# Optimization experiments

Measured on AMD Instinct MI355X. Metric: run time of the kernel, lower is better.

## Reference

```python
import jax, jax.numpy as jnp
import numpy as np
from jax import lax

EPS = 1e-5


def fps(xyz, npoint):
    # Farthest point sampling; xyz [B, N, 3] -> idx [B, npoint] (starts at point 0)
    B, N, _ = xyz.shape

    def body(carry, _):
        dist, far = carry
        c = jnp.take_along_axis(xyz, far[:, None, None], axis=1)  # [B,1,3]
        d = jnp.sum((xyz - c) ** 2, -1)                            # [B,N]
        dist = jnp.minimum(dist, d)
        nxt = jnp.argmax(dist, -1).astype(jnp.int32)
        return (dist, nxt), far

    init = (jnp.full((B, N), 1e10, xyz.dtype), jnp.zeros((B,), jnp.int32))
    _, idx = lax.scan(body, init, None, length=npoint)
    return idx.T  # [B, npoint]


def query_ball(radius, nsample, xyz, new_xyz):
    # xyz [B,N,3], new_xyz [B,S,3] -> idx [B,S,nsample]
    N = xyz.shape[1]
    sqr = jnp.sum((new_xyz[:, :, None, :] - xyz[:, None, :, :]) ** 2, -1)  # [B,S,N]
    idx = jnp.where(sqr > radius * radius, N, jnp.arange(N)[None, None, :])
    idx = jnp.sort(idx, axis=-1)[:, :, :nsample]
    # out-of-ball slots get replaced by the first in-ball index (torch repo behavior)
    return jnp.where(idx == N, idx[:, :, :1], idx)


def gather_pts(x, idx):
    # x [B,N,C], idx [B,...] -> [B,...,C]
    B = x.shape[0]
    b = jnp.arange(B).reshape((B,) + (1,) * (idx.ndim - 1))
    return x[b, idx]


def mlp_bn(x, layers):
    # x [B,S,K,C]; shared 1x1-conv MLP + training-mode BatchNorm + ReLU
    for w, g, b in layers:
        x = jnp.einsum('bskc,oc->bsko', x, w)
        mean = x.mean((0, 1, 2))
        var = x.var((0, 1, 2))  # biased, as torch BN uses for normalization
        x = jax.nn.relu((x - mean) * lax.rsqrt(var + EPS) * g + b)
    return x


def set_abstraction(xyz, points, npoint, radius, nsample, layers, group_all):
    B = xyz.shape[0]
    if group_all:
        new_xyz = jnp.zeros((B, 1, 3), xyz.dtype)
        new_points = xyz[:, None]  # [B,1,N,3] (raw xyz, no centering)
        if points is not None:
            new_points = jnp.concatenate([new_points, points[:, None]], -1)
    else:
        fidx = fps(xyz, npoint)
        new_xyz = gather_pts(xyz, fidx)                     # [B,S,3]
        idx = query_ball(radius, nsample, xyz, new_xyz)     # [B,S,K]
        grouped = gather_pts(xyz, idx) - new_xyz[:, :, None, :]
        if points is not None:
            new_points = jnp.concatenate([grouped, gather_pts(points, idx)], -1)
        else:
            new_points = grouped
    feat = mlp_bn(new_points, layers).max(2)  # max-pool over neighbors -> [B,S,C]
    return new_xyz, feat


def _forward(xyz_time, l1, l2, l3):
    B, T, N, _ = xyz_time.shape
    x = xyz_time.reshape(B * T, N, 4)
    xyz, t = x[..., :3], x[..., 3:]
    x1_xyz, x1 = set_abstraction(xyz, t, 512, 0.2, 32, l1, False)
    x2_xyz, x2 = set_abstraction(x1_xyz, x1, 128, 0.4, 64, l2, False)
    _, x3 = set_abstraction(x2_xyz, x2, None, None, None, l3, True)
    return x3.reshape(B, T, -1)


def setup_inputs() -> dict:
    key = jax.random.key(0)
    ks = jax.random.split(key, 16)
    inp = {"xyz_time": jax.random.uniform(ks[0], (2, 4, 4096, 4), jnp.float32)}
    specs = {1: [(64, 4), (64, 64), (128, 64)],
             2: [(128, 131), (128, 128), (256, 128)],
             3: [(256, 259), (512, 256), (1024, 512)]}
    i = 1
    for s, layers in specs.items():
        for j, (o, c) in enumerate(layers):
            inp[f"w{s}_{j}"] = jax.random.normal(jax.random.fold_in(ks[i], j), (o, c), jnp.float32) * 0.1
            inp[f"g{s}_{j}"] = jnp.ones((o,), jnp.float32)
            inp[f"b{s}_{j}"] = jnp.zeros((o,), jnp.float32)
        i += 1
    return inp


def reference(xyz_time, w1_0, g1_0, b1_0, w1_1, g1_1, b1_1, w1_2, g1_2, b1_2,
              w2_0, g2_0, b2_0, w2_1, g2_1, b2_1, w2_2, g2_2, b2_2,
              w3_0, g3_0, b3_0, w3_1, g3_1, b3_1, w3_2, g3_2, b3_2):
    l1 = [(w1_0, g1_0, b1_0), (w1_1, g1_1, b1_1), (w1_2, g1_2, b1_2)]
    l2 = [(w2_0, g2_0, b2_0), (w2_1, g2_1, b2_1), (w2_2, g2_2, b2_2)]
    l3 = [(w3_0, g3_0, b3_0), (w3_1, g3_1, b3_1), (w3_2, g3_2, b3_2)]
    return _forward(xyz_time, l1, l2, l3)
```

## Files before the change

kernel.cpp:

```cpp
#include <hip/hip_runtime.h>


typedef short s16x8 __attribute__((ext_vector_type(8)));
typedef float f32x4 __attribute__((ext_vector_type(4)));

__device__ __forceinline__ unsigned short f2bf_rne(float f) {
    unsigned u = __float_as_uint(f);
    u += 0x7FFFu + ((u >> 16) & 1u);
    return (unsigned short)(u >> 16);
}
__device__ __forceinline__ void f2bf_split(float v, unsigned short& hi,
                                           unsigned short& lo) {
    unsigned u = __float_as_uint(v);
    unsigned r = u + 0x7FFFu + ((u >> 16) & 1u);
    hi = (unsigned short)(r >> 16);
    float vh = __uint_as_float(r & 0xFFFF0000u);
    lo = f2bf_rne(v - vh);
}

__device__ __forceinline__ unsigned long long umax64(unsigned long long a,
                                                     unsigned long long b) {
    return a > b ? a : b;
}

__device__ __forceinline__ unsigned wred_umax63(unsigned v) {
    unsigned t;
    t = (unsigned)__builtin_amdgcn_update_dpp(0, (int)v, 0x111, 0xf, 0xf, true); if (t > v) v = t;
    t = (unsigned)__builtin_amdgcn_update_dpp(0, (int)v, 0x112, 0xf, 0xf, true); if (t > v) v = t;
    t = (unsigned)__builtin_amdgcn_update_dpp(0, (int)v, 0x114, 0xf, 0xf, true); if (t > v) v = t;
    t = (unsigned)__builtin_amdgcn_update_dpp(0, (int)v, 0x118, 0xf, 0xf, true); if (t > v) v = t;
    t = (unsigned)__builtin_amdgcn_update_dpp(0, (int)v, 0x142, 0xa, 0xf, true); if (t > v) v = t;
    t = (unsigned)__builtin_amdgcn_update_dpp(0, (int)v, 0x143, 0xc, 0xf, true); if (t > v) v = t;
    return v;
}

__device__ __forceinline__ void wave_argmax(unsigned dbits, unsigned nInv,
                                            unsigned& vmax, unsigned& iInv) {
    unsigned m = wred_umax63(dbits);
    vmax = (unsigned)__builtin_amdgcn_readlane((int)m, 63);
    unsigned cand = (dbits == vmax) ? nInv : 0u;
    unsigned im = wred_umax63(cand);
    iInv = (unsigned)__builtin_amdgcn_readlane((int)im, 63);
}

template<int NT, int ITEMS, int STRIDE>
__global__ __launch_bounds__(NT) void fps_block(
    const float* __restrict__ pts, int npoint,
    int* __restrict__ outIdx, float* __restrict__ outXyz)
{
    constexpr int N = NT * ITEMS;
    constexpr int NW = NT / 64;
    __shared__ float4 scoord[N];
    __shared__ unsigned long long wkey[2][NW];

    const int b = blockIdx.x;
    const int tid = threadIdx.x;
    const int wid = tid >> 6;
    const int lane = tid & 63;
    const float* P = pts + (size_t)b * N * STRIDE;

    float px[ITEMS], py[ITEMS], pz[ITEMS], dloc[ITEMS];
#pragma unroll
    for (int w = 0; w < ITEMS; ++w) {
        int n = tid + w * NT;
        float x, y, z;
        if (STRIDE == 4) {
            float4 v = *(const float4*)(P + (size_t)n * 4);
            x = v.x; y = v.y; z = v.z;
        } else {
            x = P[(size_t)n * STRIDE + 0];
            y = P[(size_t)n * STRIDE + 1];
            z = P[(size_t)n * STRIDE + 2];
        }
        px[w] = x; py[w] = y; pz[w] = z;
        scoord[n] = make_float4(x, y, z, 0.f);
        dloc[w] = 1e10f;
    }
    __syncthreads();
    float4 c0 = scoord[0];
    float cx = c0.x, cy = c0.y, cz = c0.z;
    int far = 0;

    for (int i = 0; i < npoint; ++i) {
        if (tid == 0) {
            outIdx[(size_t)b * npoint + i] = far;
            outXyz[((size_t)b * npoint + i) * 3 + 0] = cx;
            outXyz[((size_t)b * npoint + i) * 3 + 1] = cy;
            outXyz[((size_t)b * npoint + i) * 3 + 2] = cz;
        }
        float bestV = -1.0f;
        int bestW = 0;
#pragma unroll
        for (int w = 0; w < ITEMS; ++w) {
            float dx = __fsub_rn(px[w], cx);
            float dy = __fsub_rn(py[w], cy);
            float dz = __fsub_rn(pz[w], cz);
            float d = __fadd_rn(__fadd_rn(__fmul_rn(dx, dx), __fmul_rn(dy, dy)),
                                __fmul_rn(dz, dz));
            float dd = fminf(dloc[w], d);
            dloc[w] = dd;
            if (dd > bestV) { bestV = dd; bestW = w; }
        }
        int bestN = tid + bestW * NT;
        unsigned vmax, iInv;
        wave_argmax(__float_as_uint(bestV), 0xFFFFFFFFu ^ (unsigned)bestN,
                    vmax, iInv);
        const int par = i & 1;
        if (lane == 0)
            wkey[par][wid] = ((unsigned long long)vmax << 32) | iInv;
        __syncthreads();
        unsigned long long kb = wkey[par][0];
#pragma unroll
        for (int w2 = 1; w2 < NW; ++w2) kb = umax64(kb, wkey[par][w2]);
        far = (int)(0xFFFFFFFFu ^ (unsigned)kb);
        float4 cc = scoord[far];
        cx = cc.x; cy = cc.y; cz = cc.z;
    }
}

template<int ITEMS, int STRIDE>
__global__ __launch_bounds__(64) void fps_wave(
    const float* __restrict__ pts, int npoint,
    int* __restrict__ outIdx, float* __restrict__ outXyz)
{
    constexpr int N = 64 * ITEMS;
    __shared__ float4 scoord[N];

    const int b = blockIdx.x;
    const int tid = threadIdx.x;
    const float* P = pts + (size_t)b * N * STRIDE;

    float px[ITEMS], py[ITEMS], pz[ITEMS], dloc[ITEMS];
#pragma unroll
    for (int w = 0; w < ITEMS; ++w) {
        int n = tid + w * 64;
        float x = P[(size_t)n * STRIDE + 0];
        float y = P[(size_t)n * STRIDE + 1];
        float z = P[(size_t)n * STRIDE + 2];
        px[w] = x; py[w] = y; pz[w] = z;
        scoord[n] = make_float4(x, y, z, 0.f);
        dloc[w] = 1e10f;
    }
    __syncthreads();
    float4 c0 = scoord[0];
    float cx = c0.x, cy = c0.y, cz = c0.z;
    int far = 0;

    for (int i = 0; i < npoint; ++i) {
        if (tid == 0) {
            outIdx[(size_t)b * npoint + i] = far;
            outXyz[((size_t)b * npoint + i) * 3 + 0] = cx;
            outXyz[((size_t)b * npoint + i) * 3 + 1] = cy;
            outXyz[((size_t)b * npoint + i) * 3 + 2] = cz;
        }
        float bestV = -1.0f;
        int bestW = 0;
#pragma unroll
        for (int w = 0; w < ITEMS; ++w) {
            float dx = __fsub_rn(px[w], cx);
            float dy = __fsub_rn(py[w], cy);
            float dz = __fsub_rn(pz[w], cz);
            float d = __fadd_rn(__fadd_rn(__fmul_rn(dx, dx), __fmul_rn(dy, dy)),
                                __fmul_rn(dz, dz));
            float dd = fminf(dloc[w], d);
            dloc[w] = dd;
            if (dd > bestV) { bestV = dd; bestW = w; }
        }
        int bestN = tid + bestW * 64;
        unsigned vmax, iInv;
        wave_argmax(__float_as_uint(bestV), 0xFFFFFFFFu ^ (unsigned)bestN,
                    vmax, iInv);
        far = (int)(0xFFFFFFFFu ^ iInv);
        float4 cc = scoord[far];
        cx = cc.x; cy = cc.y; cz = cc.z;
    }
}

__global__ __launch_bounds__(256) void qb_group1(
    const float* __restrict__ xyz ,
    const float* __restrict__ ctr ,
    float* __restrict__ out )
{
    int gw = (blockIdx.x * 256 + threadIdx.x) >> 6;
    int lane = threadIdx.x & 63;
    if (gw >= 4096) return;
    int b = gw >> 9;
    const float* P = xyz + (size_t)b * 4096 * 4;
    float cx = ctr[(size_t)gw * 3 + 0];
    float cy = ctr[(size_t)gw * 3 + 1];
    float cz = ctr[(size_t)gw * 3 + 2];
    float* out0 = out + (size_t)gw * 32 * 8;
    int cnt = 0;
    float f0x = 0.f, f0y = 0.f, f0z = 0.f, f0t = 0.f;
    bool haveFirst = false;
    for (int base = 0; base < 4096 && cnt < 32; base += 64) {
        int n = base + lane;
        float4 p = *(const float4*)(P + (size_t)n * 4);
        float ex = __fsub_rn(p.x, cx);
        float ey = __fsub_rn(p.y, cy);
        float ez = __fsub_rn(p.z, cz);
        float d = __fadd_rn(__fadd_rn(__fmul_rn(ex, ex), __fmul_rn(ey, ey)),
                            __fmul_rn(ez, ez));
        bool inb = !(d > 0.04f);
        unsigned long long mask = __ballot(inb);
        if (mask) {
            if (!haveFirst) {
                int fl = (int)__builtin_ctzll(mask);
                f0x = __shfl(ex, fl); f0y = __shfl(ey, fl);
                f0z = __shfl(ez, fl); f0t = __shfl(p.w, fl);
                haveFirst = true;
            }
            if (inb) {
                int pos = cnt + __builtin_popcountll(mask & ((1ull << lane) - 1ull));
                if (pos < 32) {
                    float* o = out0 + (size_t)pos * 8;
                    *(float4*)o = make_float4(ex, ey, ez, p.w);
                    *(float4*)(o + 4) = make_float4(0.f, 0.f, 0.f, 0.f);
                }
            }
            cnt += (int)__builtin_popcountll(mask);
        }
    }
    if (cnt > 32) cnt = 32;
    for (int p2 = cnt + lane; p2 < 32; p2 += 64) {
        float* o = out0 + (size_t)p2 * 8;
        *(float4*)o = make_float4(f0x, f0y, f0z, f0t);
        *(float4*)(o + 4) = make_float4(0.f, 0.f, 0.f, 0.f);
    }
}

__global__ __launch_bounds__(256) void query_ball_kernel(
    const float* __restrict__ xyz, int stride, int N,
    const float* __restrict__ centers, int nCenters, int S,
    float r2, int nsample, int* __restrict__ outIdx)
{
    int gw = (blockIdx.x * 256 + threadIdx.x) >> 6;
    int lane = threadIdx.x & 63;
    if (gw >= nCenters) return;
    int b = gw / S;
    const float* P = xyz + (size_t)b * N * stride;
    float cx = centers[(size_t)gw * 3 + 0];
    float cy = centers[(size_t)gw * 3 + 1];
    float cz = centers[(size_t)gw * 3 + 2];
    int* out = outIdx + (size_t)gw * nsample;
    int cnt = 0;
    int firstIdx = 0;
    bool haveFirst = false;
    for (int base = 0; base < N && cnt < nsample; base += 64) {
        int n = base + lane;
        bool inb = false;
        if (n < N) {
            float dx = __fsub_rn(cx, P[(size_t)n * stride + 0]);
            float dy = __fsub_rn(cy, P[(size_t)n * stride + 1]);
            float dz = __fsub_rn(cz, P[(size_t)n * stride + 2]);
            float d = __fadd_rn(__fadd_rn(__fmul_rn(dx, dx), __fmul_rn(dy, dy)),
                                __fmul_rn(dz, dz));
            inb = !(d > r2);
        }
        unsigned long long mask = __ballot(inb);
        if (mask) {
            if (!haveFirst) { firstIdx = base + __builtin_ctzll(mask); haveFirst = true; }
            if (inb) {
                int pos = cnt + __builtin_popcountll(mask & ((1ull << lane) - 1ull));
                if (pos < nsample) out[pos] = n;
            }
            cnt += (int)__builtin_popcountll(mask);
        }
    }
    if (cnt > nsample) cnt = nsample;
    for (int p = cnt + lane; p < nsample; p += 64) out[p] = firstIdx;
}

__global__ __launch_bounds__(256) void group2_kernel(
    const float* __restrict__ xyz, const float* __restrict__ feat,
    const int* __restrict__ qb, const float* __restrict__ ctr,
    float* __restrict__ out)
{
    int i = blockIdx.x * 256 + threadIdx.x;
    if (i >= 65536 * 136) return;
    int sk = i / 136;
    int c = i - sk * 136;
    int b = sk / (128 * 64);
    int bs = sk / 64;
    int idx = qb[sk];
    idx = (idx < 0) ? 0 : (idx > 511 ? 511 : idx);
    float v = 0.f;
    if (c < 3)        v = __fsub_rn(xyz[((size_t)b * 512 + idx) * 3 + c], ctr[(size_t)bs * 3 + c]);
    else if (c < 131) v = feat[((size_t)b * 512 + idx) * 128 + (c - 3)];
    out[i] = v;
}

__global__ __launch_bounds__(256) void group3_kernel(
    const float* __restrict__ ctr2, const float* __restrict__ feat2,
    float* __restrict__ out)
{
    int i = blockIdx.x * 256 + threadIdx.x;
    if (i >= 1024 * 264) return;
    int sk = i / 264;
    int c = i - sk * 264;
    float v = 0.f;
    if (c < 3)        v = ctr2[(size_t)sk * 3 + c];
    else if (c < 259) v = feat2[(size_t)sk * 256 + (c - 3)];
    out[i] = v;
}

struct PWArgs {
    const float* w[9];
    unsigned off[9];
    int O[9], C[9], CP[9];
};
__global__ __launch_bounds__(256) void prep_w_all(
    PWArgs a, unsigned short* __restrict__ wh, unsigned short* __restrict__ wl,
    int total)
{
    int i = blockIdx.x * 256 + threadIdx.x;
    if (i >= total) return;
    int l = 0;
#pragma unroll
    for (int k = 1; k < 9; ++k) if (i >= (int)a.off[k]) l = k;
    int li = i - (int)a.off[l];
    int CP = a.CP[l];
    int o = li / CP;
    int c = li - o * CP;
    float v = (c < a.C[l]) ? a.w[l][(size_t)o * a.C[l] + c] : 0.f;
    unsigned short h, lo;
    f2bf_split(v, h, lo);
    wh[i] = h; wl[i] = lo;
}

__global__ __launch_bounds__(256) void gemm_fused(
    const float* __restrict__ X,
    const float* __restrict__ scale, const float* __restrict__ shift,
    int applyAct,
    const unsigned short* __restrict__ Bh, const unsigned short* __restrict__ Bl,
    float* __restrict__ Y, double* __restrict__ part,
    int M, int AC, int CPW, int O)
{
    constexpr int PITCH = 40;
    __shared__ __align__(16) unsigned short sAh[128 * PITCH];
    __shared__ __align__(16) unsigned short sAl[128 * PITCH];
    __shared__ __align__(16) unsigned short sBh[128 * PITCH];
    __shared__ __align__(16) unsigned short sBl[128 * PITCH];
    __shared__ float sred[2048];

    const int tid = threadIdx.x;
    const int lane = tid & 63;
    const int wid = tid >> 6;
    const int col15 = lane & 15;
    const int quad = lane >> 4;
    const int wm = (wid >> 1) * 64;
    const int wo = (wid & 1) * 64;
    const int m0 = blockIdx.x * 128;
    const int o0 = blockIdx.y * 128;
    const int YB = gridDim.x;
    const int lr = tid >> 2;
    const int lc = (tid & 3) * 8;

    f32x4 acc[4][4];
#pragma unroll
    for (int mt = 0; mt < 4; ++mt)
#pragma unroll
        for (int ot = 0; ot < 4; ++ot)
            acc[mt][ot] = {0.f, 0.f, 0.f, 0.f};

    for (int k0 = 0; k0 < CPW; k0 += 32) {
#pragma unroll
        for (int it = 0; it < 2; ++it) {
            int r = lr + it * 64;
            int c = k0 + lc;
            unsigned short h[8], l[8];
            if (c + 8 <= AC) {
                const float* xr = X + (size_t)(m0 + r) * AC + c;
                float4 v0 = *(const float4*)xr;
                float4 v1 = *(const float4*)(xr + 4);
                float vv[8] = {v0.x, v0.y, v0.z, v0.w, v1.x, v1.y, v1.z, v1.w};
#pragma unroll
                for (int j = 0; j < 8; ++j) {
                    float v = vv[j];
                    if (applyAct) v = fmaxf(v * scale[c + j] + shift[c + j], 0.f);
                    f2bf_split(v, h[j], l[j]);
                }
            } else {
#pragma unroll
                for (int j = 0; j < 8; ++j) { h[j] = 0; l[j] = 0; }
            }
            *(ushort4*)&sAh[r * PITCH + lc] = make_ushort4(h[0], h[1], h[2], h[3]);
            *(ushort4*)&sAh[r * PITCH + lc + 4] = make_ushort4(h[4], h[5], h[6], h[7]);
            *(ushort4*)&sAl[r * PITCH + lc] = make_ushort4(l[0], l[1], l[2], l[3]);
            *(ushort4*)&sAl[r * PITCH + lc + 4] = make_ushort4(l[4], l[5], l[6], l[7]);
        }
#pragma unroll
        for (int it = 0; it < 2; ++it) {
            int r = lr + it * 64;
            int c = k0 + lc;
            int o = o0 + r;
            uint4 vh = {0, 0, 0, 0}, vl = {0, 0, 0, 0};
            if (o < O && c < CPW) {
                size_t goff = (size_t)o * CPW + c;
                vh = *(const uint4*)(Bh + goff);
                vl = *(const uint4*)(Bl + goff);
            }
            *(uint4*)&sBh[r * PITCH + lc] = vh;
            *(uint4*)&sBl[r * PITCH + lc] = vl;
        }
        __syncthreads();
        s16x8 ah[4], al[4], bh[4], bl[4];
#pragma unroll
        for (int mt = 0; mt < 4; ++mt) {
            int rowoff = (wm + mt * 16 + col15) * PITCH + quad * 8;
            ah[mt] = *(const s16x8*)&sAh[rowoff];
            al[mt] = *(const s16x8*)&sAl[rowoff];
        }
#pragma unroll
        for (int ot = 0; ot < 4; ++ot) {
            int rowoff = (wo + ot * 16 + col15) * PITCH + quad * 8;
            bh[ot] = *(const s16x8*)&sBh[rowoff];
            bl[ot] = *(const s16x8*)&sBl[rowoff];
        }
#pragma unroll
        for (int mt = 0; mt < 4; ++mt)
#pragma unroll
            for (int ot = 0; ot < 4; ++ot) {
                acc[mt][ot] = __builtin_amdgcn_mfma_f32_16x16x32_bf16(
                    ah[mt], bl[ot], acc[mt][ot], 0, 0, 0);
                acc[mt][ot] = __builtin_amdgcn_mfma_f32_16x16x32_bf16(
                    al[mt], bh[ot], acc[mt][ot], 0, 0, 0);
                acc[mt][ot] = __builtin_amdgcn_mfma_f32_16x16x32_bf16(
                    ah[mt], bh[ot], acc[mt][ot], 0, 0, 0);
            }
        __syncthreads();
    }
#pragma unroll
    for (int mt = 0; mt < 4; ++mt)
#pragma unroll
        for (int ot = 0; ot < 4; ++ot) {
            int og = o0 + wo + ot * 16 + col15;
            if (og < O) {
#pragma unroll
                for (int r = 0; r < 4; ++r) {
                    int mg = m0 + wm + mt * 16 + quad * 4 + r;
                    Y[(size_t)mg * O + og] = acc[mt][ot][r];
                }
            }
        }
#pragma unroll
    for (int ot = 0; ot < 4; ++ot) {
        float s = 0.f, s2 = 0.f;
#pragma unroll
        for (int mt = 0; mt < 4; ++mt)
#pragma unroll
            for (int r = 0; r < 4; ++r) {
                float v = acc[mt][ot][r];
                s += v;
                s2 += v * v;
            }
        int slot = ((wid * 4 + quad) * 16 + col15) * 4 + ot;
        sred[slot * 2] = s;
        sred[slot * 2 + 1] = s2;
    }
    __syncthreads();
    if (tid < 128) {
        int col = tid;
        int o = o0 + col;
        if (o < O) {
            int cb = col >> 6;
            int ot = (col & 63) >> 4;
            int c15 = col & 15;
            double S = 0.0, S2 = 0.0;
#pragma unroll
            for (int wp = 0; wp < 2; ++wp) {
                int wd = cb + wp * 2;
#pragma unroll
                for (int q = 0; q < 4; ++q) {
                    int slot = ((wd * 4 + q) * 16 + c15) * 4 + ot;
                    S += (double)sred[slot * 2];
                    S2 += (double)sred[slot * 2 + 1];
                }
            }
            part[(size_t)o * YB + blockIdx.x] = S;
            part[(size_t)O * YB + (size_t)o * YB + blockIdx.x] = S2;
        }
    }
}

__global__ __launch_bounds__(256) void finalize_bn(
    const double* __restrict__ part, const float* __restrict__ g,
    const float* __restrict__ bb, float* __restrict__ scale,
    float* __restrict__ shift, int O, int YB, double invM)
{
    int o = blockIdx.x;
    int tid = threadIdx.x;
    double s = 0.0, s2 = 0.0;
    for (int yb = tid; yb < YB; yb += 256) {
        s  += part[(size_t)o * YB + yb];
        s2 += part[(size_t)O * YB + (size_t)o * YB + yb];
    }
    __shared__ double sd[512];
    sd[tid] = s;
    sd[256 + tid] = s2;
    __syncthreads();
#pragma unroll
    for (int st = 128; st > 0; st >>= 1) {
        if (tid < st) {
            sd[tid] += sd[tid + st];
            sd[256 + tid] += sd[256 + tid + st];
        }
        __syncthreads();
    }
    if (tid == 0) {
        double mean = sd[0] * invM;
        double var = sd[256] * invM - mean * mean;
        float varf = (float)var;
        if (varf < 0.f) varf = 0.f;
        float sc = g[o] * rsqrtf(varf + 1e-5f);
        scale[o] = sc;
        shift[o] = bb[o] - (float)mean * sc;
    }
}

__global__ __launch_bounds__(256) void bn_relu_max(
    const float* __restrict__ Y, const float* __restrict__ scale,
    const float* __restrict__ shift, float* __restrict__ out,
    int Stot, int K, int O)
{
    int idx = blockIdx.x * 256 + threadIdx.x;
    if (idx >= Stot * O) return;
    int s = idx / O;
    int o = idx - s * O;
    const float* base = Y + (size_t)s * K * O + o;
    float sc = scale[o], sh = shift[o];
    float mx = 0.f;
    for (int k = 0; k < K; ++k) {
        float v = base[(size_t)k * O] * sc + sh;
        v = fmaxf(v, 0.f);
        mx = fmaxf(mx, v);
    }
    out[idx] = mx;
}

extern "C" void kernel_launch(void* const* d_in, const int* in_sizes, int n_in,
                              void* d_out, int out_size, void* d_ws, size_t ws_size,
                              hipStream_t stream)
{
    const float* xin = (const float*)d_in[0];
    const float* w[9]; const float* g[9]; const float* bb[9];
    for (int i = 0; i < 9; ++i) {
        w[i]  = (const float*)d_in[1 + 3 * i];
        g[i]  = (const float*)d_in[2 + 3 * i];
        bb[i] = (const float*)d_in[3 + 3 * i];
    }

    char* base = (char*)d_ws;
    size_t off = 0;
    auto alloc = [&](size_t bytes) -> void* {
        void* p = base + off;
        off = (off + bytes + 255) & ~(size_t)255;
        return p;
    };
    const int OC[9][3] = {{64,4,8},{64,64,64},{128,64,64},
                          {128,131,136},{128,128,128},{256,128,128},
                          {256,259,264},{512,256,256},{1024,512,512}};
    size_t woff[10]; woff[0] = 0;
    for (int i = 0; i < 9; ++i) woff[i + 1] = woff[i] + (size_t)OC[i][0] * OC[i][2];

    int*    fps1   = (int*)alloc((size_t)4096 * 4);
    int*    fps2   = (int*)alloc((size_t)1024 * 4);
    int*    qb2    = (int*)alloc((size_t)65536 * 4);
    float*  nx1    = (float*)alloc((size_t)12288 * 4);
    float*  nx2    = (float*)alloc((size_t)3072 * 4);
    float*  feat1  = (float*)alloc((size_t)524288 * 4);
    float*  feat2  = (float*)alloc((size_t)262144 * 4);
    double* part   = (double*)alloc((size_t)262144 * 8);
    float*  scales = (float*)alloc((size_t)9 * 1024 * 4);
    float*  shifts = (float*)alloc((size_t)9 * 1024 * 4);
    unsigned short* WH = (unsigned short*)alloc(woff[9] * 2);
    unsigned short* WL = (unsigned short*)alloc(woff[9] * 2);
    const size_t zeroBytes = off;
    float*  XG = (float*)alloc((size_t)65536 * 136 * 4);
    float*  A  = (float*)alloc((size_t)16777216 * 4);
    if (off > ws_size) return;

    hipMemsetAsync(d_ws, 0, zeroBytes, stream);

    PWArgs pwa;
    for (int i = 0; i < 9; ++i) {
        pwa.w[i] = w[i]; pwa.off[i] = (unsigned)woff[i];
        pwa.O[i] = OC[i][0]; pwa.C[i] = OC[i][1]; pwa.CP[i] = OC[i][2];
    }
    prep_w_all<<<(int)((woff[9] + 255) / 256), 256, 0, stream>>>(pwa, WH, WL, (int)woff[9]);

    fps_block<256, 16, 4><<<8, 256, 0, stream>>>(xin, 512, fps1, nx1);
    qb_group1<<<(4096 * 64) / 256, 256, 0, stream>>>(xin, nx1, XG);

    gemm_fused<<<dim3(1024, 1), 256, 0, stream>>>(XG, nullptr, nullptr, 0, WH + woff[0], WL + woff[0], A, part, 131072, 8, 8, 64);
    finalize_bn<<<64, 256, 0, stream>>>(part, g[0], bb[0], scales + 0 * 1024, shifts + 0 * 1024, 64, 1024, 1.0 / 131072.0);
    gemm_fused<<<dim3(1024, 1), 256, 0, stream>>>(A, scales + 0 * 1024, shifts + 0 * 1024, 1, WH + woff[1], WL + woff[1], XG, part, 131072, 64, 64, 64);
    finalize_bn<<<64, 256, 0, stream>>>(part, g[1], bb[1], scales + 1 * 1024, shifts + 1 * 1024, 64, 1024, 1.0 / 131072.0);
    gemm_fused<<<dim3(1024, 1), 256, 0, stream>>>(XG, scales + 1 * 1024, shifts + 1 * 1024, 1, WH + woff[2], WL + woff[2], A, part, 131072, 64, 64, 128);
    finalize_bn<<<128, 256, 0, stream>>>(part, g[2], bb[2], scales + 2 * 1024, shifts + 2 * 1024, 128, 1024, 1.0 / 131072.0);
    bn_relu_max<<<(4096 * 128) / 256, 256, 0, stream>>>(A, scales + 2 * 1024, shifts + 2 * 1024, feat1, 4096, 32, 128);

    fps_wave<8, 3><<<8, 64, 0, stream>>>(nx1, 128, fps2, nx2);
    query_ball_kernel<<<(8 * 128 * 64) / 256, 256, 0, stream>>>(
        nx1, 3, 512, nx2, 8 * 128, 128, 0.16f, 64, qb2);
    group2_kernel<<<(65536 * 136) / 256, 256, 0, stream>>>(nx1, feat1, qb2, nx2, XG);

    gemm_fused<<<dim3(512, 1), 256, 0, stream>>>(XG, nullptr, nullptr, 0, WH + woff[3], WL + woff[3], A, part, 65536, 136, 136, 128);
    finalize_bn<<<128, 256, 0, stream>>>(part, g[3], bb[3], scales + 3 * 1024, shifts + 3 * 1024, 128, 512, 1.0 / 65536.0);
    gemm_fused<<<dim3(512, 1), 256, 0, stream>>>(A, scales + 3 * 1024, shifts + 3 * 1024, 1, WH + woff[4], WL + woff[4], XG, part, 65536, 128, 128, 128);
    finalize_bn<<<128, 256, 0, stream>>>(part, g[4], bb[4], scales + 4 * 1024, shifts + 4 * 1024, 128, 512, 1.0 / 65536.0);
    gemm_fused<<<dim3(512, 2), 256, 0, stream>>>(XG, scales + 4 * 1024, shifts + 4 * 1024, 1, WH + woff[5], WL + woff[5], A, part, 65536, 128, 128, 256);
    finalize_bn<<<256, 256, 0, stream>>>(part, g[5], bb[5], scales + 5 * 1024, shifts + 5 * 1024, 256, 512, 1.0 / 65536.0);
    bn_relu_max<<<(1024 * 256) / 256, 256, 0, stream>>>(A, scales + 5 * 1024, shifts + 5 * 1024, feat2, 1024, 64, 256);

    group3_kernel<<<(1024 * 264) / 256, 256, 0, stream>>>(nx2, feat2, XG);

    gemm_fused<<<dim3(8, 2), 256, 0, stream>>>(XG, nullptr, nullptr, 0, WH + woff[6], WL + woff[6], A, part, 1024, 264, 264, 256);
    finalize_bn<<<256, 256, 0, stream>>>(part, g[6], bb[6], scales + 6 * 1024, shifts + 6 * 1024, 256, 8, 1.0 / 1024.0);
    gemm_fused<<<dim3(8, 4), 256, 0, stream>>>(A, scales + 6 * 1024, shifts + 6 * 1024, 1, WH + woff[7], WL + woff[7], XG, part, 1024, 256, 256, 512);
    finalize_bn<<<512, 256, 0, stream>>>(part, g[7], bb[7], scales + 7 * 1024, shifts + 7 * 1024, 512, 8, 1.0 / 1024.0);
    gemm_fused<<<dim3(8, 8), 256, 0, stream>>>(XG, scales + 7 * 1024, shifts + 7 * 1024, 1, WH + woff[8], WL + woff[8], A, part, 1024, 512, 512, 1024);
    finalize_bn<<<1024, 256, 0, stream>>>(part, g[8], bb[8], scales + 8 * 1024, shifts + 8 * 1024, 1024, 8, 1.0 / 1024.0);
    bn_relu_max<<<(8 * 1024) / 256, 256, 0, stream>>>(A, scales + 8 * 1024, shifts + 8 * 1024, (float*)d_out, 8, 128, 1024);
}
```

Before: 837.9 us.

## Use packed f32 math in FPS and carry winner coordinates instead of LDS lookup

The FPS kernels now hold coordinates as float pairs and compute distances with v_pk_add/v_pk_mul, roughly halving the VALU instructions in the inner loop. Each thread also tracks the coordinates of its best point. The winning wave publishes them alongside its key (block version), or they are fetched with readlane from the winning lane (wave version), so the shared-memory coordinate table and its dependent lookup on the serial critical path go away. The risks are extra registers and select instructions for tracking coordinates, and that the inline asm can limit compiler scheduling.

```diff
diff --git a/kernel.cpp b/kernel.cpp
--- a/kernel.cpp
+++ b/kernel.cpp
@@ -3,6 +3,7 @@
 
 typedef short s16x8 __attribute__((ext_vector_type(8)));
 typedef float f32x4 __attribute__((ext_vector_type(4)));
+typedef float f32x2 __attribute__((ext_vector_type(2)));
 
 __device__ __forceinline__ unsigned short f2bf_rne(float f) {
     unsigned u = __float_as_uint(f);
@@ -18,9 +19,15 @@
     lo = f2bf_rne(v - vh);
 }
 
-__device__ __forceinline__ unsigned long long umax64(unsigned long long a,
-                                                     unsigned long long b) {
-    return a > b ? a : b;
+__device__ __forceinline__ f32x2 pk_add(f32x2 a, f32x2 b) {
+    f32x2 d;
+    asm("v_pk_add_f32 %0, %1, %2" : "=v"(d) : "v"(a), "v"(b));
+    return d;
+}
+__device__ __forceinline__ f32x2 pk_mul(f32x2 a, f32x2 b) {
+    f32x2 d;
+    asm("v_pk_mul_f32 %0, %1, %2" : "=v"(d) : "v"(a), "v"(b));
+    return d;
 }
 
 __device__ __forceinline__ unsigned wred_umax63(unsigned v) {
@@ -50,35 +57,42 @@
 {
     constexpr int N = NT * ITEMS;
     constexpr int NW = NT / 64;
-    __shared__ float4 scoord[N];
+    constexpr int PAIRS = ITEMS / 2;
     __shared__ unsigned long long wkey[2][NW];
+    __shared__ float4 wrec[2][NW];
 
     const int b = blockIdx.x;
     const int tid = threadIdx.x;
     const int wid = tid >> 6;
-    const int lane = tid & 63;
     const float* P = pts + (size_t)b * N * STRIDE;
 
-    float px[ITEMS], py[ITEMS], pz[ITEMS], dloc[ITEMS];
-#pragma unroll
-    for (int w = 0; w < ITEMS; ++w) {
-        int n = tid + w * NT;
-        float x, y, z;
+    f32x2 px[PAIRS], py[PAIRS], pz[PAIRS];
+    float dloc[ITEMS];
+#pragma unroll
+    for (int j = 0; j < PAIRS; ++j) {
+        int n0 = tid + (2 * j) * NT;
+        int n1 = tid + (2 * j + 1) * NT;
+        float x0, y0, z0, x1, y1, z1;
         if (STRIDE == 4) {
-            float4 v = *(const float4*)(P + (size_t)n * 4);
-            x = v.x; y = v.y; z = v.z;
+            float4 v0 = *(const float4*)(P + (size_t)n0 * 4);
+            float4 v1 = *(const float4*)(P + (size_t)n1 * 4);
+            x0 = v0.x; y0 = v0.y; z0 = v0.z;
+            x1 = v1.x; y1 = v1.y; z1 = v1.z;
         } else {
-            x = P[(size_t)n * STRIDE + 0];
-            y = P[(size_t)n * STRIDE + 1];
-            z = P[(size_t)n * STRIDE + 2];
-        }
-        px[w] = x; py[w] = y; pz[w] = z;
-        scoord[n] = make_float4(x, y, z, 0.f);
-        dloc[w] = 1e10f;
-    }
-    __syncthreads();
-    float4 c0 = scoord[0];
-    float cx = c0.x, cy = c0.y, cz = c0.z;
+            x0 = P[(size_t)n0 * STRIDE + 0];
+            y0 = P[(size_t)n0 * STRIDE + 1];
+            z0 = P[(size_t)n0 * STRIDE + 2];
+            x1 = P[(size_t)n1 * STRIDE + 0];
+            y1 = P[(size_t)n1 * STRIDE + 1];
+            z1 = P[(size_t)n1 * STRIDE + 2];
+        }
+        px[j] = f32x2{x0, x1};
+        py[j] = f32x2{y0, y1};
+        pz[j] = f32x2{z0, z1};
+        dloc[2 * j] = 1e10f;
+        dloc[2 * j + 1] = 1e10f;
+    }
+    float cx = P[0], cy = P[1], cz = P[2];
     int far = 0;
 
     for (int i = 0; i < npoint; ++i) {
@@ -88,33 +102,50 @@
             outXyz[((size_t)b * npoint + i) * 3 + 1] = cy;
             outXyz[((size_t)b * npoint + i) * 3 + 2] = cz;
         }
+        float ncx = -cx, ncy = -cy, ncz = -cz;
+        f32x2 c2x = {ncx, ncx}, c2y = {ncy, ncy}, c2z = {ncz, ncz};
         float bestV = -1.0f;
         int bestW = 0;
-#pragma unroll
-        for (int w = 0; w < ITEMS; ++w) {
-            float dx = __fsub_rn(px[w], cx);
-            float dy = __fsub_rn(py[w], cy);
-            float dz = __fsub_rn(pz[w], cz);
-            float d = __fadd_rn(__fadd_rn(__fmul_rn(dx, dx), __fmul_rn(dy, dy)),
-                                __fmul_rn(dz, dz));
-            float dd = fminf(dloc[w], d);
-            dloc[w] = dd;
-            if (dd > bestV) { bestV = dd; bestW = w; }
+        float bX = 0.f, bY = 0.f, bZ = 0.f;
+#pragma unroll
+        for (int j = 0; j < PAIRS; ++j) {
+            f32x2 dx = pk_add(px[j], c2x);
+            f32x2 dy = pk_add(py[j], c2y);
+            f32x2 dz = pk_add(pz[j], c2z);
+            f32x2 d = pk_add(pk_add(pk_mul(dx, dx), pk_mul(dy, dy)),
+                             pk_mul(dz, dz));
+#pragma unroll
+            for (int h = 0; h < 2; ++h) {
+                int w = 2 * j + h;
+                float dd = fminf(dloc[w], d[h]);
+                dloc[w] = dd;
+                if (dd > bestV) {
+                    bestV = dd; bestW = w;
+                    bX = px[j][h]; bY = py[j][h]; bZ = pz[j][h];
+                }
+            }
         }
         int bestN = tid + bestW * NT;
         unsigned vmax, iInv;
         wave_argmax(__float_as_uint(bestV), 0xFFFFFFFFu ^ (unsigned)bestN,
                     vmax, iInv);
         const int par = i & 1;
-        if (lane == 0)
+        if (__float_as_uint(bestV) == vmax &&
+            (0xFFFFFFFFu ^ (unsigned)bestN) == iInv) {
             wkey[par][wid] = ((unsigned long long)vmax << 32) | iInv;
+            wrec[par][wid] = make_float4(bX, bY, bZ, 0.f);
+        }
         __syncthreads();
         unsigned long long kb = wkey[par][0];
-#pragma unroll
-        for (int w2 = 1; w2 < NW; ++w2) kb = umax64(kb, wkey[par][w2]);
+        float4 rb = wrec[par][0];
+#pragma unroll
+        for (int w2 = 1; w2 < NW; ++w2) {
+            unsigned long long k2 = wkey[par][w2];
+            float4 r2 = wrec[par][w2];
+            if (k2 > kb) { kb = k2; rb = r2; }
+        }
         far = (int)(0xFFFFFFFFu ^ (unsigned)kb);
-        float4 cc = scoord[far];
-        cx = cc.x; cy = cc.y; cz = cc.z;
+        cx = rb.x; cy = rb.y; cz = rb.z;
     }
 }
 
@@ -124,26 +155,31 @@
     int* __restrict__ outIdx, float* __restrict__ outXyz)
 {
     constexpr int N = 64 * ITEMS;
-    __shared__ float4 scoord[N];
+    constexpr int PAIRS = ITEMS / 2;
 
     const int b = blockIdx.x;
     const int tid = threadIdx.x;
     const float* P = pts + (size_t)b * N * STRIDE;
 
-    float px[ITEMS], py[ITEMS], pz[ITEMS], dloc[ITEMS];
-#pragma unroll
-    for (int w = 0; w < ITEMS; ++w) {
-        int n = tid + w * 64;
-        float x = P[(size_t)n * STRIDE + 0];
-        float y = P[(size_t)n * STRIDE + 1];
-        float z = P[(size_t)n * STRIDE + 2];
-        px[w] = x; py[w] = y; pz[w] = z;
-        scoord[n] = make_float4(x, y, z, 0.f);
-        dloc[w] = 1e10f;
-    }
-    __syncthreads();
-    float4 c0 = scoord[0];
-    float cx = c0.x, cy = c0.y, cz = c0.z;
+    f32x2 px[PAIRS], py[PAIRS], pz[PAIRS];
+    float dloc[ITEMS];
+#pragma unroll
+    for (int j = 0; j < PAIRS; ++j) {
+        int n0 = tid + (2 * j) * 64;
+        int n1 = tid + (2 * j + 1) * 64;
+        float x0 = P[(size_t)n0 * STRIDE + 0];
+        float y0 = P[(size_t)n0 * STRIDE + 1];
+        float z0 = P[(size_t)n0 * STRIDE + 2];
+        float x1 = P[(size_t)n1 * STRIDE + 0];
+        float y1 = P[(size_t)n1 * STRIDE + 1];
+        float z1 = P[(size_t)n1 * STRIDE + 2];
+        px[j] = f32x2{x0, x1};
+        py[j] = f32x2{y0, y1};
+        pz[j] = f32x2{z0, z1};
+        dloc[2 * j] = 1e10f;
+        dloc[2 * j + 1] = 1e10f;
+    }
+    float cx = P[0], cy = P[1], cz = P[2];
     int far = 0;
 
     for (int i = 0; i < npoint; ++i) {
@@ -153,26 +189,41 @@
             outXyz[((size_t)b * npoint + i) * 3 + 1] = cy;
             outXyz[((size_t)b * npoint + i) * 3 + 2] = cz;
         }
+        float ncx = -cx, ncy = -cy, ncz = -cz;
+        f32x2 c2x = {ncx, ncx}, c2y = {ncy, ncy}, c2z = {ncz, ncz};
         float bestV = -1.0f;
         int bestW = 0;
-#pragma unroll
-        for (int w = 0; w < ITEMS; ++w) {
-            float dx = __fsub_rn(px[w], cx);
-            float dy = __fsub_rn(py[w], cy);
-            float dz = __fsub_rn(pz[w], cz);
-            float d = __fadd_rn(__fadd_rn(__fmul_rn(dx, dx), __fmul_rn(dy, dy)),
-                                __fmul_rn(dz, dz));
-            float dd = fminf(dloc[w], d);
-            dloc[w] = dd;
-            if (dd > bestV) { bestV = dd; bestW = w; }
+        float bX = 0.f, bY = 0.f, bZ = 0.f;
+#pragma unroll
+        for (int j = 0; j < PAIRS; ++j) {
+            f32x2 dx = pk_add(px[j], c2x);
+            f32x2 dy = pk_add(py[j], c2y);
+            f32x2 dz = pk_add(pz[j], c2z);
+            f32x2 d = pk_add(pk_add(pk_mul(dx, dx), pk_mul(dy, dy)),
+                             pk_mul(dz, dz));
+#pragma unroll
+            for (int h = 0; h < 2; ++h) {
+                int w = 2 * j + h;
+                float dd = fminf(dloc[w], d[h]);
+                dloc[w] = dd;
+                if (dd > bestV) {
+                    bestV = dd; bestW = w;
+                    bX = px[j][h]; bY = py[j][h]; bZ = pz[j][h];
+                }
+            }
         }
         int bestN = tid + bestW * 64;
         unsigned vmax, iInv;
         wave_argmax(__float_as_uint(bestV), 0xFFFFFFFFu ^ (unsigned)bestN,
                     vmax, iInv);
         far = (int)(0xFFFFFFFFu ^ iInv);
-        float4 cc = scoord[far];
-        cx = cc.x; cy = cc.y; cz = cc.z;
+        int ol = far & 63;
+        cx = __uint_as_float((unsigned)__builtin_amdgcn_readlane(
+                 (int)__float_as_uint(bX), ol));
+        cy = __uint_as_float((unsigned)__builtin_amdgcn_readlane(
+                 (int)__float_as_uint(bY), ol));
+        cz = __uint_as_float((unsigned)__builtin_amdgcn_readlane(
+                 (int)__float_as_uint(bZ), ol));
     }
 }
 
```

Measured after the change: 1.020 ms. +21.7%, slower.

## Fold weight prep into FPS1 launch and overlap FPS2 with layer-3 GEMM

Applied to the files above, without the earlier changes.

Weight bf16-split preparation now runs as extra blocks of the first FPS kernel instead of a separate launch. The second-stage farthest point sampling (single-wave kernel) now runs as extra blocks appended to the third stage-1 GEMM grid, using its shared memory. Both remove a kernel launch and let the long serial FPS loops overlap with parallel work. The trade-off is a more complex GEMM kernel signature, and the extra FPS blocks may extend the GEMM's tail.

```diff
diff --git a/kernel.cpp b/kernel.cpp
--- a/kernel.cpp
+++ b/kernel.cpp
@@ -43,15 +43,45 @@
     iInv = (unsigned)__builtin_amdgcn_readlane((int)im, 63);
 }
 
+struct PWArgs {
+    const float* w[9];
+    unsigned off[9];
+    int O[9], C[9], CP[9];
+};
+__device__ __forceinline__ void prep_w_dev(const PWArgs& a,
+                                           unsigned short* __restrict__ wh,
+                                           unsigned short* __restrict__ wl,
+                                           int i) {
+    int l = 0;
+#pragma unroll
+    for (int k = 1; k < 9; ++k) if (i >= (int)a.off[k]) l = k;
+    int li = i - (int)a.off[l];
+    int CP = a.CP[l];
+    int o = li / CP;
+    int c = li - o * CP;
+    float v = (c < a.C[l]) ? a.w[l][(size_t)o * a.C[l] + c] : 0.f;
+    unsigned short h, lo;
+    f2bf_split(v, h, lo);
+    wh[i] = h; wl[i] = lo;
+}
+
 template<int NT, int ITEMS, int STRIDE>
 __global__ __launch_bounds__(NT) void fps_block(
     const float* __restrict__ pts, int npoint,
-    int* __restrict__ outIdx, float* __restrict__ outXyz)
+    int* __restrict__ outIdx, float* __restrict__ outXyz,
+    int nFps, PWArgs pw, unsigned short* __restrict__ wh,
+    unsigned short* __restrict__ wl, int wtotal)
 {
     constexpr int N = NT * ITEMS;
     constexpr int NW = NT / 64;
     __shared__ float4 scoord[N];
     __shared__ unsigned long long wkey[2][NW];
+
+    if (blockIdx.x >= nFps) {
+        int i = (blockIdx.x - nFps) * NT + threadIdx.x;
+        if (i < wtotal) prep_w_dev(pw, wh, wl, i);
+        return;
+    }
 
     const int b = blockIdx.x;
     const int tid = threadIdx.x;
@@ -118,15 +148,13 @@
     }
 }
 
-template<int ITEMS, int STRIDE>
-__global__ __launch_bounds__(64) void fps_wave(
-    const float* __restrict__ pts, int npoint,
-    int* __restrict__ outIdx, float* __restrict__ outXyz)
-{
+__device__ void fps_wave_dev(const float* __restrict__ pts, int npoint,
+                             int* __restrict__ outIdx, float* __restrict__ outXyz,
+                             int b, float4* scoord)
+{
+    constexpr int ITEMS = 8;
+    constexpr int STRIDE = 3;
     constexpr int N = 64 * ITEMS;
-    __shared__ float4 scoord[N];
-
-    const int b = blockIdx.x;
     const int tid = threadIdx.x;
     const float* P = pts + (size_t)b * N * STRIDE;
 
@@ -141,7 +169,7 @@
         scoord[n] = make_float4(x, y, z, 0.f);
         dloc[w] = 1e10f;
     }
-    __syncthreads();
+    __threadfence_block();
     float4 c0 = scoord[0];
     float cx = c0.x, cy = c0.y, cz = c0.z;
     int far = 0;
@@ -304,37 +332,15 @@
     out[i] = v;
 }
 
-struct PWArgs {
-    const float* w[9];
-    unsigned off[9];
-    int O[9], C[9], CP[9];
-};
-__global__ __launch_bounds__(256) void prep_w_all(
-    PWArgs a, unsigned short* __restrict__ wh, unsigned short* __restrict__ wl,
-    int total)
-{
-    int i = blockIdx.x * 256 + threadIdx.x;
-    if (i >= total) return;
-    int l = 0;
-#pragma unroll
-    for (int k = 1; k < 9; ++k) if (i >= (int)a.off[k]) l = k;
-    int li = i - (int)a.off[l];
-    int CP = a.CP[l];
-    int o = li / CP;
-    int c = li - o * CP;
-    float v = (c < a.C[l]) ? a.w[l][(size_t)o * a.C[l] + c] : 0.f;
-    unsigned short h, lo;
-    f2bf_split(v, h, lo);
-    wh[i] = h; wl[i] = lo;
-}
-
 __global__ __launch_bounds__(256) void gemm_fused(
     const float* __restrict__ X,
     const float* __restrict__ scale, const float* __restrict__ shift,
     int applyAct,
     const unsigned short* __restrict__ Bh, const unsigned short* __restrict__ Bl,
     float* __restrict__ Y, double* __restrict__ part,
-    int M, int AC, int CPW, int O)
+    int M, int AC, int CPW, int O, int YBmain,
+    const float* __restrict__ fpsPts, int fpsNpoint,
+    int* __restrict__ fpsIdx, float* __restrict__ fpsXyz)
 {
     constexpr int PITCH = 40;
     __shared__ __align__(16) unsigned short sAh[128 * PITCH];
@@ -342,6 +348,13 @@
     __shared__ __align__(16) unsigned short sBh[128 * PITCH];
     __shared__ __align__(16) unsigned short sBl[128 * PITCH];
     __shared__ float sred[2048];
+
+    if ((int)blockIdx.x >= YBmain) {
+        if (threadIdx.x < 64 && fpsPts != nullptr)
+            fps_wave_dev(fpsPts, fpsNpoint, fpsIdx, fpsXyz,
+                         (int)blockIdx.x - YBmain, (float4*)sAh);
+        return;
+    }
 
     const int tid = threadIdx.x;
     const int lane = tid & 63;
@@ -352,7 +365,7 @@
     const int wo = (wid & 1) * 64;
     const int m0 = blockIdx.x * 128;
     const int o0 = blockIdx.y * 128;
-    const int YB = gridDim.x;
+    const int YB = YBmain;
     const int lr = tid >> 2;
     const int lc = (tid & 3) * 8;
 
@@ -587,39 +600,39 @@
         pwa.w[i] = w[i]; pwa.off[i] = (unsigned)woff[i];
         pwa.O[i] = OC[i][0]; pwa.C[i] = OC[i][1]; pwa.CP[i] = OC[i][2];
     }
-    prep_w_all<<<(int)((woff[9] + 255) / 256), 256, 0, stream>>>(pwa, WH, WL, (int)woff[9]);
-
-    fps_block<256, 16, 4><<<8, 256, 0, stream>>>(xin, 512, fps1, nx1);
+    const int nPrep = (int)((woff[9] + 255) / 256);
+
+    fps_block<256, 16, 4><<<8 + nPrep, 256, 0, stream>>>(
+        xin, 512, fps1, nx1, 8, pwa, WH, WL, (int)woff[9]);
     qb_group1<<<(4096 * 64) / 256, 256, 0, stream>>>(xin, nx1, XG);
 
-    gemm_fused<<<dim3(1024, 1), 256, 0, stream>>>(XG, nullptr, nullptr, 0, WH + woff[0], WL + woff[0], A, part, 131072, 8, 8, 64);
+    gemm_fused<<<dim3(1024, 1), 256, 0, stream>>>(XG, nullptr, nullptr, 0, WH + woff[0], WL + woff[0], A, part, 131072, 8, 8, 64, 1024, nullptr, 0, nullptr, nullptr);
     finalize_bn<<<64, 256, 0, stream>>>(part, g[0], bb[0], scales + 0 * 1024, shifts + 0 * 1024, 64, 1024, 1.0 / 131072.0);
-    gemm_fused<<<dim3(1024, 1), 256, 0, stream>>>(A, scales + 0 * 1024, shifts + 0 * 1024, 1, WH + woff[1], WL + woff[1], XG, part, 131072, 64, 64, 64);
+    gemm_fused<<<dim3(1024, 1), 256, 0, stream>>>(A, scales + 0 * 1024, shifts + 0 * 1024, 1, WH + woff[1], WL + woff[1], XG, part, 131072, 64, 64, 64, 1024, nullptr, 0, nullptr, nullptr);
     finalize_bn<<<64, 256, 0, stream>>>(part, g[1], bb[1], scales + 1 * 1024, shifts + 1 * 1024, 64, 1024, 1.0 / 131072.0);
-    gemm_fused<<<dim3(1024, 1), 256, 0, stream>>>(XG, scales + 1 * 1024, shifts + 1 * 1024, 1, WH + woff[2], WL + woff[2], A, part, 131072, 64, 64, 128);
+    gemm_fused<<<dim3(1024 + 8, 1), 256, 0, stream>>>(XG, scales + 1 * 1024, shifts + 1 * 1024, 1, WH + woff[2], WL + woff[2], A, part, 131072, 64, 64, 128, 1024, nx1, 128, fps2, nx2);
     finalize_bn<<<128, 256, 0, stream>>>(part, g[2], bb[2], scales + 2 * 1024, shifts + 2 * 1024, 128, 1024, 1.0 / 131072.0);
     bn_relu_max<<<(4096 * 128) / 256, 256, 0, stream>>>(A, scales + 2 * 1024, shifts + 2 * 1024, feat1, 4096, 32, 128);
 
-    fps_wave<8, 3><<<8, 64, 0, stream>>>(nx1, 128, fps2, nx2);
     query_ball_kernel<<<(8 * 128 * 64) / 256, 256, 0, stream>>>(
         nx1, 3, 512, nx2, 8 * 128, 128, 0.16f, 64, qb2);
     group2_kernel<<<(65536 * 136) / 256, 256, 0, stream>>>(nx1, feat1, qb2, nx2, XG);
 
-    gemm_fused<<<dim3(512, 1), 256, 0, stream>>>(XG, nullptr, nullptr, 0, WH + woff[3], WL + woff[3], A, part, 65536, 136, 136, 128);
+    gemm_fused<<<dim3(512, 1), 256, 0, stream>>>(XG, nullptr, nullptr, 0, WH + woff[3], WL + woff[3], A, part, 65536, 136, 136, 128, 512, nullptr, 0, nullptr, nullptr);
     finalize_bn<<<128, 256, 0, stream>>>(part, g[3], bb[3], scales + 3 * 1024, shifts + 3 * 1024, 128, 512, 1.0 / 65536.0);
-    gemm_fused<<<dim3(512, 1), 256, 0, stream>>>(A, scales + 3 * 1024, shifts + 3 * 1024, 1, WH + woff[4], WL + woff[4], XG, part, 65536, 128, 128, 128);
+    gemm_fused<<<dim3(512, 1), 256, 0, stream>>>(A, scales + 3 * 1024, shifts + 3 * 1024, 1, WH + woff[4], WL + woff[4], XG, part, 65536, 128, 128, 128, 512, nullptr, 0, nullptr, nullptr);
     finalize_bn<<<128, 256, 0, stream>>>(part, g[4], bb[4], scales + 4 * 1024, shifts + 4 * 1024, 128, 512, 1.0 / 65536.0);
-    gemm_fused<<<dim3(512, 2), 256, 0, stream>>>(XG, scales + 4 * 1024, shifts + 4 * 1024, 1, WH + woff[5], WL + woff[5], A, part, 65536, 128, 128, 256);
+    gemm_fused<<<dim3(512, 2), 256, 0, stream>>>(XG, scales + 4 * 1024, shifts + 4 * 1024, 1, WH + woff[5], WL + woff[5], A, part, 65536, 128, 128, 256, 512, nullptr, 0, nullptr, nullptr);
     finalize_bn<<<256, 256, 0, stream>>>(part, g[5], bb[5], scales + 5 * 1024, shifts + 5 * 1024, 256, 512, 1.0 / 65536.0);
     bn_relu_max<<<(1024 * 256) / 256, 256, 0, stream>>>(A, scales + 5 * 1024, shifts + 5 * 1024, feat2, 1024, 64, 256);
 
     group3_kernel<<<(1024 * 264) / 256, 256, 0, stream>>>(nx2, feat2, XG);
 
-    gemm_fused<<<dim3(8, 2), 256, 0, stream>>>(XG, nullptr, nullptr, 0, WH + woff[6], WL + woff[6], A, part, 1024, 264, 264, 256);
+    gemm_fused<<<dim3(8, 2), 256, 0, stream>>>(XG, nullptr, nullptr, 0, WH + woff[6], WL + woff[6], A, part, 1024, 264, 264, 256, 8, nullptr, 0, nullptr, nullptr);
     finalize_bn<<<256, 256, 0, stream>>>(part, g[6], bb[6], scales + 6 * 1024, shifts + 6 * 1024, 256, 8, 1.0 / 1024.0);
-    gemm_fused<<<dim3(8, 4), 256, 0, stream>>>(A, scales + 6 * 1024, shifts + 6 * 1024, 1, WH + woff[7], WL + woff[7], XG, part, 1024, 256, 256, 512);
+    gemm_fused<<<dim3(8, 4), 256, 0, stream>>>(A, scales + 6 * 1024, shifts + 6 * 1024, 1, WH + woff[7], WL + woff[7], XG, part, 1024, 256, 256, 512, 8, nullptr, 0, nullptr, nullptr);
     finalize_bn<<<512, 256, 0, stream>>>(part, g[7], bb[7], scales + 7 * 1024, shifts + 7 * 1024, 512, 8, 1.0 / 1024.0);
-    gemm_fused<<<dim3(8, 8), 256, 0, stream>>>(XG, scales + 7 * 1024, shifts + 7 * 1024, 1, WH + woff[8], WL + woff[8], A, part, 1024, 512, 512, 1024);
+    gemm_fused<<<dim3(8, 8), 256, 0, stream>>>(XG, scales + 7 * 1024, shifts + 7 * 1024, 1, WH + woff[8], WL + woff[8], A, part, 1024, 512, 512, 1024, 8, nullptr, 0, nullptr, nullptr);
     finalize_bn<<<1024, 256, 0, stream>>>(part, g[8], bb[8], scales + 8 * 1024, shifts + 8 * 1024, 1024, 8, 1.0 / 1024.0);
     bn_relu_max<<<(8 * 1024) / 256, 256, 0, stream>>>(A, scales + 8 * 1024, shifts + 8 * 1024, (float*)d_out, 8, 128, 1024);
 }
```

New measurement: 826.1 us. No clear change (-1.4%).
